# Kernel tuning notes

Measured on AMD Instinct MI355X. Metric: run time of the kernel, lower is better.

Reference implementation:

```python
import jax, jax.numpy as jnp
import numpy as np

K = 1024          # num_embeddings
D = 256           # embedding_dim
COMMITMENT = 0.25


def setup_inputs() -> dict:
    key = jax.random.key(0)
    k1, k2, k3 = jax.random.split(key, 3)
    return {
        "inputs": jax.random.normal(k1, (64, 2048, D), dtype=jnp.float32),
        "pre_w": jax.random.normal(k2, (D, D), dtype=jnp.float32) / jnp.sqrt(jnp.float32(D)),
        "pre_b": jnp.zeros((D,), dtype=jnp.float32),
        "emb": jax.random.uniform(k3, (K, D), dtype=jnp.float32, minval=-1.0, maxval=1.0),
    }


def reference(inputs, pre_w, pre_b, emb):
    # flatten to tokens [N, D] and apply pre_linear
    flat = inputs.reshape(-1, D)
    f = flat @ pre_w.T + pre_b                       # [N, D]
    # squared euclidean distances to codebook: ||f||^2 + ||e||^2 - 2 f e^T
    distances = (jnp.sum(f * f, axis=1, keepdims=True)
                 + jnp.sum(emb * emb, axis=1)
                 - 2.0 * (f @ emb.T))                # [N, K]
    idx = jnp.argmin(distances, axis=1)              # [N]
    encodings = jax.nn.one_hot(idx, K, dtype=inputs.dtype)  # [N, K]
    # quantized = encodings @ emb  ==  gather rows of codebook
    quantized = emb[idx].reshape(inputs.shape)       # [B, S, D]
    # commitment loss (quantized detached)
    e_latent_loss = jnp.mean((jax.lax.stop_gradient(quantized) - inputs) ** 2)
    loss = COMMITMENT * e_latent_loss
    # straight-through estimator
    quantized_st = inputs + jax.lax.stop_gradient(quantized - inputs)
    avg_probs = jnp.mean(encodings, axis=0)          # [K]
    perplexity = jnp.exp(-jnp.sum(avg_probs * jnp.log(avg_probs + 1e-10)))
    return loss, quantized_st, perplexity, encodings
```

## Files before the change

### kernel.cpp

```cpp
#include <hip/hip_runtime.h>
#include <math.h>

#define NTOK 131072
#define DDIM 256
#define KCB  1024

static constexpr size_t O_Q = 1;
static constexpr size_t O_P = 1 + (size_t)NTOK * DDIM;
static constexpr size_t O_E = O_P + 1;
static constexpr size_t SCRATCH_FHI = O_E + 2;
static constexpr size_t SCRATCH_FLO = SCRATCH_FHI + (size_t)NTOK * DDIM / 2;
static constexpr size_t SCRATCH_EHI = SCRATCH_FLO + (size_t)NTOK * DDIM / 2;
static constexpr size_t SCRATCH_ELO = SCRATCH_EHI + (size_t)KCB * DDIM / 2;
static constexpr size_t SCRATCH_FLG = SCRATCH_ELO + (size_t)KCB * DDIM / 2;

static constexpr size_t WS_IDX   = 0;
static constexpr size_t WS_EN    = (size_t)NTOK * 4;
static constexpr size_t WS_CNT   = WS_EN + (size_t)KCB * 4;
static constexpr size_t WS_ACC   = WS_CNT + (size_t)KCB * 4;
static constexpr size_t WS_FLAGN = WS_ACC + 8;

#define TS 128
#define KC 32
#define LDSROW 36

#define EPS_GAP 0.0625f

typedef short bf16x8 __attribute__((ext_vector_type(8)));
typedef float f32x4  __attribute__((ext_vector_type(4)));
typedef unsigned short us4v __attribute__((ext_vector_type(4)));

__device__ __forceinline__ unsigned short f2bf(float x) {
    unsigned u = __float_as_uint(x);
    return (unsigned short)((u + 0x7FFFu + ((u >> 16) & 1u)) >> 16);
}
__device__ __forceinline__ float bf2f(unsigned short h) {
    return __uint_as_float(((unsigned)h) << 16);
}

__global__ __launch_bounds__(64) void k_enorm(const float* __restrict__ emb,
                                              float* __restrict__ enorm,
                                              unsigned short* __restrict__ ehi,
                                              unsigned short* __restrict__ elo) {
    int k = blockIdx.x;
    float4 v = reinterpret_cast<const float4*>(emb)[(size_t)k * 64 + threadIdx.x];
    float s = v.x * v.x + v.y * v.y + v.z * v.z + v.w * v.w;

    float xs[4] = {v.x, v.y, v.z, v.w};
    us4v hv, lv;
#pragma unroll
    for (int i = 0; i < 4; ++i) {
        unsigned short h = f2bf(xs[i]);
        hv[i] = h;
        lv[i] = f2bf(xs[i] - bf2f(h));
    }
    *reinterpret_cast<us4v*>(ehi + (size_t)k * DDIM + threadIdx.x * 4) = hv;
    *reinterpret_cast<us4v*>(elo + (size_t)k * DDIM + threadIdx.x * 4) = lv;

    for (int off = 32; off >= 1; off >>= 1) s += __shfl_down(s, off, 64);
    if (threadIdx.x == 0) enorm[k] = s;
}

__device__ __forceinline__ void tile_fma(const float* __restrict__ sA,
                                         const float* __restrict__ sB,
                                         int tx, int ty,
                                         float acc[8][8]) {
#pragma unroll 1
    for (int is = 0; is < 8; ++is) {
        float4 bv[8];
#pragma unroll
        for (int c = 0; c < 8; ++c)
            bv[c] = *reinterpret_cast<const float4*>(&sB[(tx + 16 * c) * LDSROW + is * 4]);
#pragma unroll
        for (int j = 0; j < 8; ++j) {
            float4 a = *reinterpret_cast<const float4*>(&sA[(ty + 16 * j) * LDSROW + is * 4]);
#pragma unroll
            for (int c = 0; c < 8; ++c)
                acc[j][c] += a.x * bv[c].x + a.y * bv[c].y + a.z * bv[c].z + a.w * bv[c].w;
        }
    }
}

__global__ __launch_bounds__(256, 2) void k_gemm1(const float* __restrict__ x,
                                                  const float* __restrict__ w,
                                                  const float* __restrict__ b,
                                                  unsigned short* __restrict__ fhi,
                                                  unsigned short* __restrict__ flo) {
    __shared__ float sA[TS * LDSROW];
    __shared__ float sB[TS * LDSROW];
    const int tid = threadIdx.x;
    const int tx = tid & 15, ty = tid >> 4;
    const int tb = blockIdx.x * TS;
    const int db = blockIdx.y * TS;

    float acc[8][8];
#pragma unroll
    for (int j = 0; j < 8; ++j)
#pragma unroll
        for (int c = 0; c < 8; ++c) acc[j][c] = 0.f;

    const float4* x4 = reinterpret_cast<const float4*>(x);
    const float4* w4 = reinterpret_cast<const float4*>(w);

    const int pr = tid >> 3, pi = tid & 7;
    float4 pa[4], pb[4];
#pragma unroll
    for (int l0 = 0; l0 < 4; ++l0) {
        int row = l0 * 32 + pr;
        pa[l0] = x4[(size_t)(tb + row) * 64 + pi];
        pb[l0] = w4[(size_t)(db + row) * 64 + pi];
    }

#pragma unroll 1
    for (int kc = 0; kc < DDIM / KC; ++kc) {
        __syncthreads();
#pragma unroll
        for (int l0 = 0; l0 < 4; ++l0) {
            int row = l0 * 32 + pr;
            *reinterpret_cast<float4*>(&sA[row * LDSROW + pi * 4]) = pa[l0];
            *reinterpret_cast<float4*>(&sB[row * LDSROW + pi * 4]) = pb[l0];
        }
        __syncthreads();
        if (kc < DDIM / KC - 1) {
#pragma unroll
            for (int l0 = 0; l0 < 4; ++l0) {
                int row = l0 * 32 + pr;
                pa[l0] = x4[(size_t)(tb + row) * 64 + (kc + 1) * 8 + pi];
                pb[l0] = w4[(size_t)(db + row) * 64 + (kc + 1) * 8 + pi];
            }
        }
        tile_fma(sA, sB, tx, ty, acc);
    }

    float bias[8];
#pragma unroll
    for (int c = 0; c < 8; ++c) bias[c] = b[db + tx + 16 * c];
#pragma unroll
    for (int j = 0; j < 8; ++j) {
        size_t rowo = (size_t)(tb + ty + 16 * j) * DDIM + db;
#pragma unroll
        for (int c = 0; c < 8; ++c) {
            float v = acc[j][c] + bias[c];
            int col = tx + 16 * c;
            unsigned short h = f2bf(v);
            fhi[rowo + col] = h;
            flo[rowo + col] = f2bf(v - bf2f(h));
        }
    }
}

__global__ __launch_bounds__(256, 2) void k_argmin_mfma(
        const unsigned short* __restrict__ fhi, const unsigned short* __restrict__ flo,
        const unsigned short* __restrict__ ehi, const unsigned short* __restrict__ elo,
        const float* __restrict__ enorm,
        int* __restrict__ idx, int* __restrict__ flaglist, unsigned* __restrict__ flagn) {
    __shared__ bf16x8 sB[1024];
    const int tid  = threadIdx.x;
    const int lane = tid & 63;
    const int wv   = tid >> 6;
    const int row  = lane & 15;
    const int kg   = lane >> 4;
    const int tok0 = blockIdx.x * 128 + wv * 32;

    bf16x8 ah[2][8], al[2][8];
#pragma unroll
    for (int m = 0; m < 2; ++m)
#pragma unroll
        for (int kk = 0; kk < 8; ++kk) {
            size_t off = (size_t)(tok0 + m * 16 + row) * DDIM + kk * 32 + kg * 8;
            ah[m][kk] = *reinterpret_cast<const bf16x8*>(fhi + off);
            al[m][kk] = *reinterpret_cast<const bf16x8*>(flo + off);
        }

    float bd1[2][4], bd2[2][4];
    int   bk1[2][4];
#pragma unroll
    for (int m = 0; m < 2; ++m)
#pragma unroll
        for (int r = 0; r < 4; ++r) { bd1[m][r] = 3.4e38f; bd2[m][r] = 3.4e38f; bk1[m][r] = 0; }

    const int sxr = row & 7;
    const int pcode = (tid >> 5) & 15, pch = tid & 31;
    const bool plo = tid >= 512 / 1;

    bf16x8 st[4];
#pragma unroll
    for (int i = 0; i < 4; ++i) {
        int c = i * 256 + tid;
        int code = (c >> 5) & 15, ch = c & 31;
        const unsigned short* src = (c < 512) ? ehi : elo;
        st[i] = *reinterpret_cast<const bf16x8*>(src + (size_t)code * DDIM + ch * 8);
    }

#pragma unroll 1
    for (int nt = 0; nt < KCB / 16; ++nt) {
        __syncthreads();
#pragma unroll
        for (int i = 0; i < 4; ++i) {
            int c = i * 256 + tid;
            int code = (c >> 5) & 15, ch = c & 31;
            sB[((c < 512) ? 0 : 512) + code * 32 + (ch ^ (code & 7))] = st[i];
        }
        __syncthreads();
        if (nt < KCB / 16 - 1) {
#pragma unroll
            for (int i = 0; i < 4; ++i) {
                int c = i * 256 + tid;
                int code = (c >> 5) & 15, ch = c & 31;
                const unsigned short* src = (c < 512) ? ehi : elo;
                st[i] = *reinterpret_cast<const bf16x8*>(
                    src + (size_t)((nt + 1) * 16 + code) * DDIM + ch * 8);
            }
        }

        f32x4 acc0a = {0.f, 0.f, 0.f, 0.f}, acc0b = {0.f, 0.f, 0.f, 0.f};
        f32x4 acc1a = {0.f, 0.f, 0.f, 0.f}, acc1b = {0.f, 0.f, 0.f, 0.f};
#pragma unroll
        for (int kk = 0; kk < 8; ++kk) {
            int slot = row * 32 + (((kk * 4) + kg) ^ sxr);
            bf16x8 bh = sB[slot];
            bf16x8 bl = sB[512 + slot];
            acc0a = __builtin_amdgcn_mfma_f32_16x16x32_bf16(ah[0][kk], bh, acc0a, 0, 0, 0);
            acc1a = __builtin_amdgcn_mfma_f32_16x16x32_bf16(ah[1][kk], bh, acc1a, 0, 0, 0);
            acc0b = __builtin_amdgcn_mfma_f32_16x16x32_bf16(al[0][kk], bh, acc0b, 0, 0, 0);
            acc1b = __builtin_amdgcn_mfma_f32_16x16x32_bf16(al[1][kk], bh, acc1b, 0, 0, 0);
            acc0b = __builtin_amdgcn_mfma_f32_16x16x32_bf16(ah[0][kk], bl, acc0b, 0, 0, 0);
            acc1b = __builtin_amdgcn_mfma_f32_16x16x32_bf16(ah[1][kk], bl, acc1b, 0, 0, 0);
        }

        int code = nt * 16 + row;
        float en = enorm[code];
#pragma unroll
        for (int r = 0; r < 4; ++r) {
            float d0 = en - 2.f * (acc0a[r] + acc0b[r]);
            float d1 = en - 2.f * (acc1a[r] + acc1b[r]);
            if (d0 < bd1[0][r]) { bd2[0][r] = bd1[0][r]; bd1[0][r] = d0; bk1[0][r] = code; }
            else if (d0 < bd2[0][r]) bd2[0][r] = d0;
            if (d1 < bd1[1][r]) { bd2[1][r] = bd1[1][r]; bd1[1][r] = d1; bk1[1][r] = code; }
            else if (d1 < bd2[1][r]) bd2[1][r] = d1;
        }
    }

#pragma unroll
    for (int m = 0; m < 2; ++m)
#pragma unroll
        for (int r = 0; r < 4; ++r) {
            float v1 = bd1[m][r], v2 = bd2[m][r];
            int k1 = bk1[m][r];
#pragma unroll
            for (int msk = 1; msk < 16; msk <<= 1) {
                float o1 = __shfl_xor(v1, msk, 16);
                float o2 = __shfl_xor(v2, msk, 16);
                int   ok = __shfl_xor(k1, msk, 16);
                if (o1 < v1 || (o1 == v1 && ok < k1)) { v2 = fminf(v1, o2); v1 = o1; k1 = ok; }
                else                                  { v2 = fminf(v2, o1); }
            }
            if (row == 0) {
                int t = tok0 + m * 16 + kg * 4 + r;
                idx[t] = k1;
                if (v2 - v1 < EPS_GAP) {
                    unsigned p = atomicAdd(flagn, 1u);
                    flaglist[p] = t;
                }
            }
        }
}

__global__ __launch_bounds__(256) void k_rescore(const float* __restrict__ x,
                                                 const float* __restrict__ w,
                                                 const float* __restrict__ bias,
                                                 const float* __restrict__ emb,
                                                 const float* __restrict__ enorm,
                                                 const int* __restrict__ flaglist,
                                                 const unsigned* __restrict__ flagn,
                                                 int* __restrict__ idx) {
    __shared__ float sx[DDIM];
    __shared__ float sf[DDIM];
    __shared__ float swd[4];
    __shared__ int   swk[4];
    const int tid = threadIdx.x;
    const unsigned n = *flagn;
    for (unsigned ii = blockIdx.x; ii < n; ii += gridDim.x) {
        const int t = flaglist[ii];
        __syncthreads();
        sx[tid] = x[(size_t)t * DDIM + tid];
        __syncthreads();
        const float4* wr = reinterpret_cast<const float4*>(w + (size_t)tid * DDIM);
        float fd = bias[tid];
#pragma unroll 8
        for (int q = 0; q < 64; ++q) {
            float4 wv = wr[q];
            float4 xv = *reinterpret_cast<const float4*>(&sx[q * 4]);
            fd += wv.x * xv.x + wv.y * xv.y + wv.z * xv.z + wv.w * xv.w;
        }
        sf[tid] = fd;
        __syncthreads();
        float bd = 3.4e38f;
        int   bk = 0;
#pragma unroll 1
        for (int j = 0; j < 4; ++j) {
            int k = j * 256 + tid;
            const float4* er = reinterpret_cast<const float4*>(emb + (size_t)k * DDIM);
            float dot = 0.f;
#pragma unroll 8
            for (int q = 0; q < 64; ++q) {
                float4 ev = er[q];
                float4 fv = *reinterpret_cast<const float4*>(&sf[q * 4]);
                dot += ev.x * fv.x + ev.y * fv.y + ev.z * fv.z + ev.w * fv.w;
            }
            float d = enorm[k] - 2.f * dot;
            if (d < bd || (d == bd && k < bk)) { bd = d; bk = k; }
        }
        for (int m = 1; m < 64; m <<= 1) {
            float od = __shfl_xor(bd, m, 64);
            int   ok = __shfl_xor(bk, m, 64);
            if (od < bd || (od == bd && ok < bk)) { bd = od; bk = ok; }
        }
        if ((tid & 63) == 0) { swd[tid >> 6] = bd; swk[tid >> 6] = bk; }
        __syncthreads();
        if (tid == 0) {
            for (int w2 = 1; w2 < 4; ++w2)
                if (swd[w2] < bd || (swd[w2] == bd && swk[w2] < bk)) { bd = swd[w2]; bk = swk[w2]; }
            idx[t] = bk;
        }
    }
}

__global__ __launch_bounds__(256) void k_out(const float* __restrict__ x,
                                             const float* __restrict__ emb,
                                             const int* __restrict__ idx,
                                             float* __restrict__ out,
                                             unsigned* __restrict__ counts,
                                             double* __restrict__ lossacc) {
    const int tid = threadIdx.x;
    const int tb = blockIdx.x * 64;
    __shared__ int   sidx[64];
    __shared__ float wsum[4];
    if (tid < 64) sidx[tid] = idx[tb + tid];
    __syncthreads();

    const float4* x4 = reinterpret_cast<const float4*>(x);
    const float4* e4 = reinterpret_cast<const float4*>(emb);
    float local = 0.f;
#pragma unroll
    for (int it = 0; it < 16; ++it) {
        int l = it * 256 + tid;
        int tok = l >> 6, q = l & 63;
        int t = tb + tok;
        int id = sidx[tok];
        if (q == 0) atomicAdd(&counts[id], 1u);
        float4 xv = x4[(size_t)t * 64 + q];
        float4 ev = e4[(size_t)id * 64 + q];
        size_t o = O_Q + (size_t)t * DDIM + (size_t)q * 4;
        out[o] = ev.x; out[o + 1] = ev.y; out[o + 2] = ev.z; out[o + 3] = ev.w;
        float dx = ev.x - xv.x, dy = ev.y - xv.y, dz = ev.z - xv.z, dw = ev.w - xv.w;
        local += dx * dx + dy * dy + dz * dz + dw * dw;
    }
    for (int off = 32; off >= 1; off >>= 1) local += __shfl_down(local, off, 64);
    if ((tid & 63) == 0) wsum[tid >> 6] = local;
    __syncthreads();
    if (tid == 0)
        atomicAdd(lossacc, (double)(wsum[0] + wsum[1] + wsum[2] + wsum[3]));

#pragma unroll 1
    for (int r = 0; r < 64; ++r) {
        int id = sidx[r];
        float* rb = out + O_E + (size_t)(tb + r) * KCB;
        int hot = id >> 1, sub = id & 1;
#pragma unroll
        for (int i = 0; i < 2; ++i) {
            int q2 = i * 256 + tid;
            float2 v = make_float2(0.f, 0.f);
            if (q2 == hot) { if (sub) v.y = 1.f; else v.x = 1.f; }
            *reinterpret_cast<float2*>(rb + (size_t)q2 * 2) = v;
        }
    }
}

__global__ __launch_bounds__(1024) void k_final(const unsigned* __restrict__ counts,
                                                const double* __restrict__ lossacc,
                                                float* __restrict__ out) {
    int tid = threadIdx.x;
    double p = (double)counts[tid] / (double)NTOK;
    double term = p * log(p + 1e-10);
    for (int off = 32; off >= 1; off >>= 1) term += __shfl_down(term, off, 64);
    __shared__ double sw[16];
    if ((tid & 63) == 0) sw[tid >> 6] = term;
    __syncthreads();
    if (tid == 0) {
        double s = 0.0;
        for (int i = 0; i < 16; ++i) s += sw[i];
        out[O_P] = (float)exp(-s);
        out[0]   = (float)(0.25 * lossacc[0] / ((double)NTOK * (double)DDIM));
    }
}

extern "C" void kernel_launch(void* const* d_in, const int* in_sizes, int n_in,
                              void* d_out, int out_size, void* d_ws, size_t ws_size,
                              hipStream_t stream) {
    const float* x   = (const float*)d_in[0];
    const float* w   = (const float*)d_in[1];
    const float* b   = (const float*)d_in[2];
    const float* emb = (const float*)d_in[3];
    float* out = (float*)d_out;

    int*      idx    = (int*)((char*)d_ws + WS_IDX);
    float*    enorm  = (float*)((char*)d_ws + WS_EN);
    unsigned* counts = (unsigned*)((char*)d_ws + WS_CNT);
    double*   acc    = (double*)((char*)d_ws + WS_ACC);
    unsigned* flagn  = (unsigned*)((char*)d_ws + WS_FLAGN);

    unsigned short* fhi      = (unsigned short*)(out + SCRATCH_FHI);
    unsigned short* flo      = (unsigned short*)(out + SCRATCH_FLO);
    unsigned short* ehi      = (unsigned short*)(out + SCRATCH_EHI);
    unsigned short* elo      = (unsigned short*)(out + SCRATCH_ELO);
    int*            flaglist = (int*)(out + SCRATCH_FLG);

    hipMemsetAsync((char*)d_ws + WS_CNT, 0, (size_t)KCB * 4 + 16, stream);

    k_enorm      <<<KCB,                        64,  0, stream>>>(emb, enorm, ehi, elo);
    k_gemm1      <<<dim3(NTOK / TS, DDIM / TS), 256, 0, stream>>>(x, w, b, fhi, flo);
    k_argmin_mfma<<<NTOK / 128,                 256, 0, stream>>>(fhi, flo, ehi, elo, enorm,
                                                                 idx, flaglist, flagn);
    k_rescore    <<<128,                        256, 0, stream>>>(x, w, b, emb, enorm,
                                                                 flaglist, flagn, idx);
    k_out        <<<NTOK / 64,                  256, 0, stream>>>(x, emb, idx, out, counts, acc);
    k_final      <<<1,                          1024, 0, stream>>>(counts, acc, out);
}
```

Baseline: 1.788 ms.

## Store fp32 pre-linear output and batch rescoring of flagged tokens in groups of 16

```diff
diff --git a/kernel.cpp b/kernel.cpp
--- a/kernel.cpp
+++ b/kernel.cpp
@@ -8,11 +8,12 @@
 static constexpr size_t O_Q = 1;
 static constexpr size_t O_P = 1 + (size_t)NTOK * DDIM;
 static constexpr size_t O_E = O_P + 1;
-static constexpr size_t SCRATCH_FHI = O_E + 2;
-static constexpr size_t SCRATCH_FLO = SCRATCH_FHI + (size_t)NTOK * DDIM / 2;
-static constexpr size_t SCRATCH_EHI = SCRATCH_FLO + (size_t)NTOK * DDIM / 2;
-static constexpr size_t SCRATCH_ELO = SCRATCH_EHI + (size_t)KCB * DDIM / 2;
-static constexpr size_t SCRATCH_FLG = SCRATCH_ELO + (size_t)KCB * DDIM / 2;
+static constexpr size_t SCRATCH_F_OFF = O_E + 2;
+static constexpr size_t SCRATCH_FHI   = SCRATCH_F_OFF + (size_t)NTOK * DDIM;
+static constexpr size_t SCRATCH_FLO   = SCRATCH_FHI + (size_t)NTOK * DDIM / 2;
+static constexpr size_t SCRATCH_EHI   = SCRATCH_FLO + (size_t)NTOK * DDIM / 2;
+static constexpr size_t SCRATCH_ELO   = SCRATCH_EHI + (size_t)KCB * DDIM / 2;
+static constexpr size_t SCRATCH_FLG   = SCRATCH_ELO + (size_t)KCB * DDIM / 2;
 
 static constexpr size_t WS_IDX   = 0;
 static constexpr size_t WS_EN    = (size_t)NTOK * 4;
@@ -84,6 +85,7 @@
 __global__ __launch_bounds__(256, 2) void k_gemm1(const float* __restrict__ x,
                                                   const float* __restrict__ w,
                                                   const float* __restrict__ b,
+                                                  float* __restrict__ f,
                                                   unsigned short* __restrict__ fhi,
                                                   unsigned short* __restrict__ flo) {
     __shared__ float sA[TS * LDSROW];
@@ -142,6 +144,7 @@
         for (int c = 0; c < 8; ++c) {
             float v = acc[j][c] + bias[c];
             int col = tx + 16 * c;
+            f[rowo + col] = v;
             unsigned short h = f2bf(v);
             fhi[rowo + col] = h;
             flo[rowo + col] = f2bf(v - bf2f(h));
@@ -180,8 +183,6 @@
         for (int r = 0; r < 4; ++r) { bd1[m][r] = 3.4e38f; bd2[m][r] = 3.4e38f; bk1[m][r] = 0; }
 
     const int sxr = row & 7;
-    const int pcode = (tid >> 5) & 15, pch = tid & 31;
-    const bool plo = tid >= 512 / 1;
 
     bf16x8 st[4];
 #pragma unroll
@@ -266,62 +267,87 @@
         }
 }
 
-__global__ __launch_bounds__(256) void k_rescore(const float* __restrict__ x,
-                                                 const float* __restrict__ w,
-                                                 const float* __restrict__ bias,
+__global__ __launch_bounds__(256) void k_rescore(const float* __restrict__ f,
                                                  const float* __restrict__ emb,
                                                  const float* __restrict__ enorm,
                                                  const int* __restrict__ flaglist,
                                                  const unsigned* __restrict__ flagn,
                                                  int* __restrict__ idx) {
-    __shared__ float sx[DDIM];
-    __shared__ float sf[DDIM];
-    __shared__ float swd[4];
-    __shared__ int   swk[4];
+    __shared__ float sf[16 * DDIM];
+    __shared__ int   stok[16];
+    __shared__ float swd[4 * 16];
+    __shared__ int   swk[4 * 16];
     const int tid = threadIdx.x;
     const unsigned n = *flagn;
-    for (unsigned ii = blockIdx.x; ii < n; ii += gridDim.x) {
-        const int t = flaglist[ii];
-        __syncthreads();
-        sx[tid] = x[(size_t)t * DDIM + tid];
-        __syncthreads();
-        const float4* wr = reinterpret_cast<const float4*>(w + (size_t)tid * DDIM);
-        float fd = bias[tid];
-#pragma unroll 8
+    const f32x4* f4 = reinterpret_cast<const f32x4*>(f);
+    const float4* e4 = reinterpret_cast<const float4*>(emb);
+    f32x4* sf4 = reinterpret_cast<f32x4*>(sf);
+
+    float en[4];
+#pragma unroll
+    for (int c = 0; c < 4; ++c) en[c] = enorm[tid + 256 * c];
+
+#pragma unroll 1
+    for (unsigned base = blockIdx.x * 16u; base < n; base += (unsigned)gridDim.x * 16u) {
+        const int m = (int)min(16u, n - base);
+        __syncthreads();
+        if (tid < 16) stok[tid] = flaglist[base + min(tid, m - 1)];
+        __syncthreads();
+#pragma unroll
+        for (int i = 0; i < 4; ++i) {
+            int t = i * 4 + (tid >> 6), q = tid & 63;
+            sf4[t * 64 + q] = f4[(size_t)stok[t] * 64 + q];
+        }
+        __syncthreads();
+
+        float dot[4][16];
+#pragma unroll
+        for (int c = 0; c < 4; ++c)
+#pragma unroll
+            for (int t = 0; t < 16; ++t) dot[c][t] = 0.f;
+
+#pragma unroll 1
         for (int q = 0; q < 64; ++q) {
-            float4 wv = wr[q];
-            float4 xv = *reinterpret_cast<const float4*>(&sx[q * 4]);
-            fd += wv.x * xv.x + wv.y * xv.y + wv.z * xv.z + wv.w * xv.w;
-        }
-        sf[tid] = fd;
-        __syncthreads();
-        float bd = 3.4e38f;
-        int   bk = 0;
-#pragma unroll 1
-        for (int j = 0; j < 4; ++j) {
-            int k = j * 256 + tid;
-            const float4* er = reinterpret_cast<const float4*>(emb + (size_t)k * DDIM);
-            float dot = 0.f;
-#pragma unroll 8
-            for (int q = 0; q < 64; ++q) {
-                float4 ev = er[q];
-                float4 fv = *reinterpret_cast<const float4*>(&sf[q * 4]);
-                dot += ev.x * fv.x + ev.y * fv.y + ev.z * fv.z + ev.w * fv.w;
-            }
-            float d = enorm[k] - 2.f * dot;
-            if (d < bd || (d == bd && k < bk)) { bd = d; bk = k; }
-        }
-        for (int m = 1; m < 64; m <<= 1) {
-            float od = __shfl_xor(bd, m, 64);
-            int   ok = __shfl_xor(bk, m, 64);
-            if (od < bd || (od == bd && ok < bk)) { bd = od; bk = ok; }
-        }
-        if ((tid & 63) == 0) { swd[tid >> 6] = bd; swk[tid >> 6] = bk; }
-        __syncthreads();
-        if (tid == 0) {
-            for (int w2 = 1; w2 < 4; ++w2)
-                if (swd[w2] < bd || (swd[w2] == bd && swk[w2] < bk)) { bd = swd[w2]; bk = swk[w2]; }
-            idx[t] = bk;
+            float4 ev[4];
+#pragma unroll
+            for (int c = 0; c < 4; ++c)
+                ev[c] = e4[(size_t)(tid + 256 * c) * 64 + q];
+#pragma unroll
+            for (int t = 0; t < 16; ++t) {
+                f32x4 fv = sf4[t * 64 + q];
+#pragma unroll
+                for (int c = 0; c < 4; ++c)
+                    dot[c][t] += ev[c].x * fv[0] + ev[c].y * fv[1]
+                               + ev[c].z * fv[2] + ev[c].w * fv[3];
+            }
+        }
+
+#pragma unroll 1
+        for (int t = 0; t < 16; ++t) {
+            float bd = 3.4e38f;
+            int   bk = 0x7fffffff;
+#pragma unroll
+            for (int c = 0; c < 4; ++c) {
+                float d = en[c] - 2.f * dot[c][t];
+                int   k = tid + 256 * c;
+                if (d < bd || (d == bd && k < bk)) { bd = d; bk = k; }
+            }
+            for (int msk = 1; msk < 64; msk <<= 1) {
+                float od = __shfl_xor(bd, msk, 64);
+                int   ok = __shfl_xor(bk, msk, 64);
+                if (od < bd || (od == bd && ok < bk)) { bd = od; bk = ok; }
+            }
+            if ((tid & 63) == 0) { swd[(tid >> 6) * 16 + t] = bd; swk[(tid >> 6) * 16 + t] = bk; }
+        }
+        __syncthreads();
+        if (tid < m) {
+            float bd = swd[tid]; int bk = swk[tid];
+#pragma unroll
+            for (int w2 = 1; w2 < 4; ++w2) {
+                float od = swd[w2 * 16 + tid]; int ok = swk[w2 * 16 + tid];
+                if (od < bd || (od == bd && ok < bk)) { bd = od; bk = ok; }
+            }
+            idx[stok[tid]] = bk;
         }
     }
 }
@@ -410,6 +436,7 @@
     double*   acc    = (double*)((char*)d_ws + WS_ACC);
     unsigned* flagn  = (unsigned*)((char*)d_ws + WS_FLAGN);
 
+    float*          scratchF = out + SCRATCH_F_OFF;
     unsigned short* fhi      = (unsigned short*)(out + SCRATCH_FHI);
     unsigned short* flo      = (unsigned short*)(out + SCRATCH_FLO);
     unsigned short* ehi      = (unsigned short*)(out + SCRATCH_EHI);
@@ -419,10 +446,10 @@
     hipMemsetAsync((char*)d_ws + WS_CNT, 0, (size_t)KCB * 4 + 16, stream);
 
     k_enorm      <<<KCB,                        64,  0, stream>>>(emb, enorm, ehi, elo);
-    k_gemm1      <<<dim3(NTOK / TS, DDIM / TS), 256, 0, stream>>>(x, w, b, fhi, flo);
+    k_gemm1      <<<dim3(NTOK / TS, DDIM / TS), 256, 0, stream>>>(x, w, b, scratchF, fhi, flo);
     k_argmin_mfma<<<NTOK / 128,                 256, 0, stream>>>(fhi, flo, ehi, elo, enorm,
                                                                  idx, flaglist, flagn);
-    k_rescore    <<<128,                        256, 0, stream>>>(x, w, b, emb, enorm,
+    k_rescore    <<<512,                        256, 0, stream>>>(scratchF, emb, enorm,
                                                                  flaglist, flagn, idx);
     k_out        <<<NTOK / 64,                  256, 0, stream>>>(x, emb, idx, out, counts, acc);
     k_final      <<<1,                          1024, 0, stream>>>(counts, acc, out);
```

Result: faster. 1.481 ms (-17.2%).
